# Performance work log

Measured on AMD Instinct MI355X. Metric: run time of the kernel, lower is better.

Reference implementation:

```python
import jax, jax.numpy as jnp
import numpy as np

TIMESCALE = 10.0   # NeuralODE init kwarg
N_MAX = 48         # static upper bound on number of constant-size Dopri5 steps
B, D, H = 8192, 128, 128


def _mlp(y, W1, b1, W2, b2):
    # autonomous dynamics f(x): tanh MLP, applied along last dim
    return jnp.tanh(y @ W1 + b1) @ W2 + b2


def _dopri5_step(y, dt, f):
    # classic Dormand-Prince 5(4) tableau; autonomous f, so c_i unused
    k1 = f(y)
    k2 = f(y + dt * (1.0 / 5.0 * k1))
    k3 = f(y + dt * (3.0 / 40.0 * k1 + 9.0 / 40.0 * k2))
    k4 = f(y + dt * (44.0 / 45.0 * k1 - 56.0 / 15.0 * k2 + 32.0 / 9.0 * k3))
    k5 = f(y + dt * (19372.0 / 6561.0 * k1 - 25360.0 / 2187.0 * k2
                     + 64448.0 / 6561.0 * k3 - 212.0 / 729.0 * k4))
    k6 = f(y + dt * (9017.0 / 3168.0 * k1 - 355.0 / 33.0 * k2
                     + 46732.0 / 5247.0 * k3 + 49.0 / 176.0 * k4
                     - 5103.0 / 18656.0 * k5))
    return y + dt * (35.0 / 384.0 * k1 + 500.0 / 1113.0 * k3
                     + 125.0 / 192.0 * k4 - 2187.0 / 6784.0 * k5
                     + 11.0 / 84.0 * k6)


def _initial_step_size(y0, f0, f, order=4, rtol=1.4e-8, atol=1.4e-8):
    # faithful port of NeuralODE.initial_step_size (Hairer heuristic)
    scale = atol + jnp.abs(y0) * rtol
    d0 = jnp.linalg.norm(y0 / scale)
    d1 = jnp.linalg.norm(f0 / scale)
    h0 = jnp.where((d0 < 1e-5) | (d1 < 1e-5), 1e-6, 0.01 * d0 / d1)
    y1 = y0 + h0 * f0
    f1 = f(y1)
    d2 = jnp.linalg.norm((f1 - f0) / scale) / h0
    h1 = jnp.where((d1 <= 1e-15) & (d2 <= 1e-15),
                   jnp.maximum(1e-6, h0 * 1e-3),
                   (0.01 / (d1 + d2)) ** (1.0 / (order + 1.0)))
    return jnp.minimum(100.0 * h0, h1)


def setup_inputs() -> dict:
    key = jax.random.key(0)
    k0, k1, k2 = jax.random.split(key, 3)
    x = jax.random.normal(k0, (B, D), jnp.float32)
    W1 = jax.random.normal(k1, (D, H), jnp.float32) * (1.0 / D ** 0.5)
    b1 = jnp.zeros((H,), jnp.float32)
    W2 = jax.random.normal(k2, (H, D), jnp.float32) * (1.0 / H ** 0.5)
    b2 = jnp.zeros((D,), jnp.float32)
    t = jnp.ones((1,), jnp.float32)
    return {"t": t, "x": x, "W1": W1, "b1": b1, "W2": W2, "b2": b2}


def reference(t, x, W1, b1, W2, b2):
    f = lambda y: _mlp(y, W1, b1, W2, b2)
    # dt0 from the first state row, exactly as the original (x[0, :])
    dt0 = _initial_step_size(x[0], f(x[0]), f)
    T = t[0] / TIMESCALE  # linspace(0, t/timescale, 2) -> ts = [0, T]

    # diffrax default ConstantStepSize: fixed-dt Dopri5 until t reaches T.
    # Static-length scan with dt clamped to the remaining interval; once
    # t == T, dt == 0 and the step is skipped via lax.cond.
    step = jax.checkpoint(
        lambda y, dt: jax.lax.cond(dt > 0.0,
                                   lambda a: _dopri5_step(a, dt, f),
                                   lambda a: a, y))

    def body(carry, _):
        tt, y = carry
        dt = jnp.clip(T - tt, 0.0, dt0)
        return (tt + dt, step(y, dt)), None

    (_, yT), _ = jax.lax.scan(body, (jnp.zeros((), jnp.float32), x), None,
                              length=N_MAX)
    # SaveAt(ts=[0, T]) -> ys has leading axis n_samples=2
    return jnp.stack([x, yT])
```

## Files before the change

### kernel.cpp

```cpp
#include <hip/hip_runtime.h>


typedef __attribute__((ext_vector_type(8))) short short8;
typedef __attribute__((ext_vector_type(4))) float f32x4;

#define SL 136

__device__ __forceinline__ short f2bf(float f) {
  union { float f; unsigned u; } v; v.f = f;
  return (short)((v.u + 0x8000u) >> 16);
}

__device__ __forceinline__ float fast_tanh(float x) {
  float e = __expf(2.0f * x);
  return 1.0f - __fdividef(2.0f, e + 1.0f);
}

__global__ __launch_bounds__(512, 4)
void node_kernel(const float* __restrict__ tptr, const float* __restrict__ x,
                 const float* __restrict__ W1, const float* __restrict__ b1,
                 const float* __restrict__ W2, const float* __restrict__ b2,
                 float* __restrict__ out) {
  const int tid  = threadIdx.x;
  const int lane = tid & 63;
  const int ct   = tid >> 6;
  const int q    = lane >> 4;
  const int colL = lane & 15;
  const int n    = ct * 16 + colL;
  const int blockRow = blockIdx.x * 16;

  __shared__ short A1[16][SL];
  __shared__ short A2[16][SL];
  __shared__ float sred[512];
  __shared__ float spart[4][128];
  __shared__ float srowY[128], srowH[128], srowF[128], srowY2[128], srowF2[128], sscale[128];

  short8 w1f[4], w2f[4];
  const float b1c = b1[n], b2c = b2[n];
#pragma unroll
  for (int kt = 0; kt < 4; ++kt) {
    short8 v1, v2;
#pragma unroll
    for (int j = 0; j < 8; ++j) {
      const int k = kt * 32 + q * 8 + j;
      v1[j] = f2bf(W1[k * 128 + n]);
      v2[j] = f2bf(W2[k * 128 + n]);
    }
    w1f[kt] = v1; w2f[kt] = v2;
  }

  auto block_sum = [&](float v) -> float {
    sred[tid] = v;
    __syncthreads();
    if (tid < 64) {
      float s = 0.f;
#pragma unroll
      for (int i = 0; i < 8; ++i) s += sred[tid + 64 * i];
#pragma unroll
      for (int o = 32; o > 0; o >>= 1) s += __shfl_down(s, o, 64);
      if (tid == 0) sred[0] = s;
    }
    __syncthreads();
    float r = sred[0];
    __syncthreads();
    return r;
  };

  auto mlp_layer = [&](const float* vin, const float* Wg, const float* bg,
                       float* vout, bool dotanh) {
    const int col = tid & 127, part = tid >> 7;
    float s = 0.f;
    const float* wp = Wg + (part * 32) * 128 + col;
#pragma unroll 8
    for (int j = 0; j < 32; ++j) s += vin[part * 32 + j] * wp[j * 128];
    spart[part][col] = s;
    __syncthreads();
    if (tid < 128) {
      float a = bg[tid] + spart[0][tid] + spart[1][tid] + spart[2][tid] + spart[3][tid];
      vout[tid] = dotanh ? fast_tanh(a) : a;
    }
    __syncthreads();
  };

  if (tid < 128) srowY[tid] = x[tid];
  __syncthreads();
  mlp_layer(srowY, W1, b1, srowH, true);
  mlp_layer(srowH, W2, b2, srowF, false);
  float t0 = 0.f, t1 = 0.f;
  if (tid < 128) {
    float sc = 1.4e-8f + fabsf(srowY[tid]) * 1.4e-8f;
    sscale[tid] = sc;
    float a = srowY[tid] / sc; t0 = a * a;
    float bq = srowF[tid] / sc; t1 = bq * bq;
  }
  float d0 = sqrtf(block_sum(t0));
  float d1 = sqrtf(block_sum(t1));
  float h0 = (d0 < 1e-5f || d1 < 1e-5f) ? 1e-6f : 0.01f * d0 / d1;
  if (tid < 128) srowY2[tid] = srowY[tid] + h0 * srowF[tid];
  __syncthreads();
  mlp_layer(srowY2, W1, b1, srowH, true);
  mlp_layer(srowH, W2, b2, srowF2, false);
  float t2 = 0.f;
  if (tid < 128) { float a = (srowF2[tid] - srowF[tid]) / sscale[tid]; t2 = a * a; }
  float d2 = sqrtf(block_sum(t2)) / h0;
  float h1 = (d1 <= 1e-15f && d2 <= 1e-15f) ? fmaxf(1e-6f, h0 * 1e-3f)
                                            : powf(0.01f / (d1 + d2), 0.2f);
  const float dt0v = fminf(100.f * h0, h1);

  f32x4 yr;
#pragma unroll
  for (int r = 0; r < 4; ++r) yr[r] = x[(blockRow + q * 4 + r) * 128 + n];

  short* wr1 = &A1[q * 4][n];
  short* wr2 = &A2[q * 4][n];
  const short* rd1 = &A1[colL][q * 8];
  const short* rd2 = &A2[colL][q * 8];

  auto evalF = [&](f32x4 yin) -> f32x4 {
#pragma unroll
    for (int r = 0; r < 4; ++r) wr1[r * SL] = f2bf(yin[r]);
    __syncthreads();
    f32x4 acc = {b1c, b1c, b1c, b1c};
#pragma unroll
    for (int kt = 0; kt < 4; ++kt)
      acc = __builtin_amdgcn_mfma_f32_16x16x32_bf16(
          *(const short8*)(rd1 + kt * 32), w1f[kt], acc, 0, 0, 0);
#pragma unroll
    for (int r = 0; r < 4; ++r) wr2[r * SL] = f2bf(fast_tanh(acc[r]));
    __syncthreads();
    f32x4 accF = {b2c, b2c, b2c, b2c};
#pragma unroll
    for (int kt = 0; kt < 4; ++kt)
      accF = __builtin_amdgcn_mfma_f32_16x16x32_bf16(
          *(const short8*)(rd2 + kt * 32), w2f[kt], accF, 0, 0, 0);
    return accF;
  };

  const float T = tptr[0] / 10.0f;
  float tt = 0.f;

#pragma unroll 1
  for (int it = 0; it < 48; ++it) {
    float dt = fminf(fmaxf(T - tt, 0.f), dt0v);
    if (dt > 0.f) {
      f32x4 k1 = evalF(yr);
      f32x4 k2 = evalF(yr + dt * (0.2f * k1));
      f32x4 k3 = evalF(yr + dt * (0.075f * k1 + 0.225f * k2));
      f32x4 k4 = evalF(yr + dt * (0.9777777777777777f * k1 - 3.7333333333333334f * k2
                                + 3.5555555555555554f * k3));
      f32x4 k5 = evalF(yr + dt * (2.9525986892242035f * k1 - 11.595793324188385f * k2
                                + 9.822892851699436f * k3 - 0.2908093278463649f * k4));
      f32x4 k6 = evalF(yr + dt * (2.8462752525252526f * k1 - 10.757575757575758f * k2
                                + 8.906422717743473f * k3 + 0.2784090909090909f * k4
                                - 0.27351165254237287f * k5));
      yr = yr + dt * (0.0911458333333333f * k1 + 0.449236298292902f * k3
                    + 0.6510416666666666f * k4 - 0.32237617924528303f * k5
                    + 0.13095238095238096f * k6);
    }
    tt += dt;
  }

  {
    const float4* x4 = (const float4*)(x + blockRow * 128);
    float4* o4 = (float4*)(out + blockRow * 128);
    o4[tid] = x4[tid];
    float* oy = out + 8192 * 128;
#pragma unroll
    for (int r = 0; r < 4; ++r)
      oy[(blockRow + q * 4 + r) * 128 + n] = yr[r];
  }
}

extern "C" void kernel_launch(void* const* d_in, const int* in_sizes, int n_in,
                              void* d_out, int out_size, void* d_ws, size_t ws_size,
                              hipStream_t stream) {
  const float* t  = (const float*)d_in[0];
  const float* x  = (const float*)d_in[1];
  const float* W1 = (const float*)d_in[2];
  const float* b1 = (const float*)d_in[3];
  const float* W2 = (const float*)d_in[4];
  const float* b2 = (const float*)d_in[5];
  float* out = (float*)d_out;
  node_kernel<<<dim3(512), dim3(512), 0, stream>>>(t, x, W1, b1, W2, b2, out);
}
```

Before: 168.3 us.

## Halve block size, give each wave two feature tiles, and transpose MFMA operands

```diff
diff --git a/kernel.cpp b/kernel.cpp
--- a/kernel.cpp
+++ b/kernel.cpp
@@ -11,51 +11,59 @@
   return (short)((v.u + 0x8000u) >> 16);
 }
 
+__device__ __forceinline__ unsigned pack2bf(float lo, float hi) {
+  union { float f; unsigned u; } a, b; a.f = lo; b.f = hi;
+  return __builtin_amdgcn_perm(b.u + 0x8000u, a.u + 0x8000u, 0x07060302u);
+}
+
 __device__ __forceinline__ float fast_tanh(float x) {
   float e = __expf(2.0f * x);
   return 1.0f - __fdividef(2.0f, e + 1.0f);
 }
 
-__global__ __launch_bounds__(512, 4)
+__global__ __launch_bounds__(256, 2)
 void node_kernel(const float* __restrict__ tptr, const float* __restrict__ x,
                  const float* __restrict__ W1, const float* __restrict__ b1,
                  const float* __restrict__ W2, const float* __restrict__ b2,
                  float* __restrict__ out) {
   const int tid  = threadIdx.x;
   const int lane = tid & 63;
-  const int ct   = tid >> 6;
+  const int w    = tid >> 6;
   const int q    = lane >> 4;
-  const int colL = lane & 15;
-  const int n    = ct * 16 + colL;
+  const int mL   = lane & 15;
   const int blockRow = blockIdx.x * 16;
 
-  __shared__ short A1[16][SL];
-  __shared__ short A2[16][SL];
-  __shared__ float sred[512];
-  __shared__ float spart[4][128];
+  __shared__ short Yb[16 * SL];
+  __shared__ short Tb[16 * SL];
+  __shared__ float sred[256];
+  __shared__ float spart[2][128];
   __shared__ float srowY[128], srowH[128], srowF[128], srowY2[128], srowF2[128], sscale[128];
 
-  short8 w1f[4], w2f[4];
-  const float b1c = b1[n], b2c = b2[n];
-#pragma unroll
-  for (int kt = 0; kt < 4; ++kt) {
-    short8 v1, v2;
-#pragma unroll
-    for (int j = 0; j < 8; ++j) {
-      const int k = kt * 32 + q * 8 + j;
-      v1[j] = f2bf(W1[k * 128 + n]);
-      v2[j] = f2bf(W2[k * 128 + n]);
-    }
-    w1f[kt] = v1; w2f[kt] = v2;
+  short8 w1t[2][4], w2t[2][4];
+  f32x4 b1v[2], b2v[2];
+#pragma unroll
+  for (int s = 0; s < 2; ++s) {
+    const int ft = (2 * w + s) * 16;
+#pragma unroll
+    for (int r = 0; r < 4; ++r) { b1v[s][r] = b1[ft + q * 4 + r]; b2v[s][r] = b2[ft + q * 4 + r]; }
+#pragma unroll
+    for (int kt = 0; kt < 4; ++kt) {
+      short8 v1, v2;
+#pragma unroll
+      for (int j = 0; j < 8; ++j) {
+        const int k = kt * 32 + q * 8 + j;
+        v1[j] = f2bf(W1[k * 128 + ft + mL]);
+        v2[j] = f2bf(W2[k * 128 + ft + mL]);
+      }
+      w1t[s][kt] = v1; w2t[s][kt] = v2;
+    }
   }
 
   auto block_sum = [&](float v) -> float {
     sred[tid] = v;
     __syncthreads();
     if (tid < 64) {
-      float s = 0.f;
-#pragma unroll
-      for (int i = 0; i < 8; ++i) s += sred[tid + 64 * i];
+      float s = sred[tid] + sred[tid + 64] + sred[tid + 128] + sred[tid + 192];
 #pragma unroll
       for (int o = 32; o > 0; o >>= 1) s += __shfl_down(s, o, 64);
       if (tid == 0) sred[0] = s;
@@ -70,13 +78,13 @@
                        float* vout, bool dotanh) {
     const int col = tid & 127, part = tid >> 7;
     float s = 0.f;
-    const float* wp = Wg + (part * 32) * 128 + col;
+    const float* wp = Wg + (part * 64) * 128 + col;
 #pragma unroll 8
-    for (int j = 0; j < 32; ++j) s += vin[part * 32 + j] * wp[j * 128];
+    for (int j = 0; j < 64; ++j) s += vin[part * 64 + j] * wp[j * 128];
     spart[part][col] = s;
     __syncthreads();
     if (tid < 128) {
-      float a = bg[tid] + spart[0][tid] + spart[1][tid] + spart[2][tid] + spart[3][tid];
+      float a = bg[tid] + spart[0][tid] + spart[1][tid];
       vout[tid] = dotanh ? fast_tanh(a) : a;
     }
     __syncthreads();
@@ -107,55 +115,90 @@
                                             : powf(0.01f / (d1 + d2), 0.2f);
   const float dt0v = fminf(100.f * h0, h1);
 
-  f32x4 yr;
-#pragma unroll
-  for (int r = 0; r < 4; ++r) yr[r] = x[(blockRow + q * 4 + r) * 128 + n];
-
-  short* wr1 = &A1[q * 4][n];
-  short* wr2 = &A2[q * 4][n];
-  const short* rd1 = &A1[colL][q * 8];
-  const short* rd2 = &A2[colL][q * 8];
-
-  auto evalF = [&](f32x4 yin) -> f32x4 {
-#pragma unroll
-    for (int r = 0; r < 4; ++r) wr1[r * SL] = f2bf(yin[r]);
-    __syncthreads();
-    f32x4 acc = {b1c, b1c, b1c, b1c};
-#pragma unroll
-    for (int kt = 0; kt < 4; ++kt)
-      acc = __builtin_amdgcn_mfma_f32_16x16x32_bf16(
-          *(const short8*)(rd1 + kt * 32), w1f[kt], acc, 0, 0, 0);
-#pragma unroll
-    for (int r = 0; r < 4; ++r) wr2[r * SL] = f2bf(fast_tanh(acc[r]));
-    __syncthreads();
-    f32x4 accF = {b2c, b2c, b2c, b2c};
-#pragma unroll
-    for (int kt = 0; kt < 4; ++kt)
-      accF = __builtin_amdgcn_mfma_f32_16x16x32_bf16(
-          *(const short8*)(rd2 + kt * 32), w2f[kt], accF, 0, 0, 0);
-    return accF;
+  f32x4 yr[2];
+#pragma unroll
+  for (int s = 0; s < 2; ++s)
+    yr[s] = *(const f32x4*)&x[(blockRow + mL) * 128 + (2 * w + s) * 16 + q * 4];
+
+  const int rowOff = mL * SL;
+  const int wrOff0 = rowOff + (2 * w) * 16 + q * 4;
+  const int wrOff1 = wrOff0 + 16;
+  const int rdOff  = rowOff + q * 8;
+
+  auto evalF = [&](const f32x4* yin, f32x4* kout) {
+    *(uint2*)&Yb[wrOff0] = uint2{pack2bf(yin[0][0], yin[0][1]), pack2bf(yin[0][2], yin[0][3])};
+    *(uint2*)&Yb[wrOff1] = uint2{pack2bf(yin[1][0], yin[1][1]), pack2bf(yin[1][2], yin[1][3])};
+    __syncthreads();
+    f32x4 acc0 = b1v[0], acc1 = b1v[1];
+    short8 rb0 = *(const short8*)&Yb[rdOff];
+    short8 rb1 = *(const short8*)&Yb[rdOff + 32];
+    short8 rb2 = *(const short8*)&Yb[rdOff + 64];
+    short8 rb3 = *(const short8*)&Yb[rdOff + 96];
+    acc0 = __builtin_amdgcn_mfma_f32_16x16x32_bf16(w1t[0][0], rb0, acc0, 0, 0, 0);
+    acc1 = __builtin_amdgcn_mfma_f32_16x16x32_bf16(w1t[1][0], rb0, acc1, 0, 0, 0);
+    acc0 = __builtin_amdgcn_mfma_f32_16x16x32_bf16(w1t[0][1], rb1, acc0, 0, 0, 0);
+    acc1 = __builtin_amdgcn_mfma_f32_16x16x32_bf16(w1t[1][1], rb1, acc1, 0, 0, 0);
+    acc0 = __builtin_amdgcn_mfma_f32_16x16x32_bf16(w1t[0][2], rb2, acc0, 0, 0, 0);
+    acc1 = __builtin_amdgcn_mfma_f32_16x16x32_bf16(w1t[1][2], rb2, acc1, 0, 0, 0);
+    acc0 = __builtin_amdgcn_mfma_f32_16x16x32_bf16(w1t[0][3], rb3, acc0, 0, 0, 0);
+    acc1 = __builtin_amdgcn_mfma_f32_16x16x32_bf16(w1t[1][3], rb3, acc1, 0, 0, 0);
+    *(uint2*)&Tb[wrOff0] = uint2{pack2bf(fast_tanh(acc0[0]), fast_tanh(acc0[1])),
+                                 pack2bf(fast_tanh(acc0[2]), fast_tanh(acc0[3]))};
+    *(uint2*)&Tb[wrOff1] = uint2{pack2bf(fast_tanh(acc1[0]), fast_tanh(acc1[1])),
+                                 pack2bf(fast_tanh(acc1[2]), fast_tanh(acc1[3]))};
+    __syncthreads();
+    f32x4 accF0 = b2v[0], accF1 = b2v[1];
+    short8 tb0 = *(const short8*)&Tb[rdOff];
+    short8 tb1 = *(const short8*)&Tb[rdOff + 32];
+    short8 tb2 = *(const short8*)&Tb[rdOff + 64];
+    short8 tb3 = *(const short8*)&Tb[rdOff + 96];
+    accF0 = __builtin_amdgcn_mfma_f32_16x16x32_bf16(w2t[0][0], tb0, accF0, 0, 0, 0);
+    accF1 = __builtin_amdgcn_mfma_f32_16x16x32_bf16(w2t[1][0], tb0, accF1, 0, 0, 0);
+    accF0 = __builtin_amdgcn_mfma_f32_16x16x32_bf16(w2t[0][1], tb1, accF0, 0, 0, 0);
+    accF1 = __builtin_amdgcn_mfma_f32_16x16x32_bf16(w2t[1][1], tb1, accF1, 0, 0, 0);
+    accF0 = __builtin_amdgcn_mfma_f32_16x16x32_bf16(w2t[0][2], tb2, accF0, 0, 0, 0);
+    accF1 = __builtin_amdgcn_mfma_f32_16x16x32_bf16(w2t[1][2], tb2, accF1, 0, 0, 0);
+    accF0 = __builtin_amdgcn_mfma_f32_16x16x32_bf16(w2t[0][3], tb3, accF0, 0, 0, 0);
+    accF1 = __builtin_amdgcn_mfma_f32_16x16x32_bf16(w2t[1][3], tb3, accF1, 0, 0, 0);
+    kout[0] = accF0; kout[1] = accF1;
   };
 
   const float T = tptr[0] / 10.0f;
   float tt = 0.f;
+  f32x4 k1[2], k2[2], k3[2], k4[2], k5[2], k6[2], yv[2];
 
 #pragma unroll 1
   for (int it = 0; it < 48; ++it) {
     float dt = fminf(fmaxf(T - tt, 0.f), dt0v);
     if (dt > 0.f) {
-      f32x4 k1 = evalF(yr);
-      f32x4 k2 = evalF(yr + dt * (0.2f * k1));
-      f32x4 k3 = evalF(yr + dt * (0.075f * k1 + 0.225f * k2));
-      f32x4 k4 = evalF(yr + dt * (0.9777777777777777f * k1 - 3.7333333333333334f * k2
-                                + 3.5555555555555554f * k3));
-      f32x4 k5 = evalF(yr + dt * (2.9525986892242035f * k1 - 11.595793324188385f * k2
-                                + 9.822892851699436f * k3 - 0.2908093278463649f * k4));
-      f32x4 k6 = evalF(yr + dt * (2.8462752525252526f * k1 - 10.757575757575758f * k2
-                                + 8.906422717743473f * k3 + 0.2784090909090909f * k4
-                                - 0.27351165254237287f * k5));
-      yr = yr + dt * (0.0911458333333333f * k1 + 0.449236298292902f * k3
-                    + 0.6510416666666666f * k4 - 0.32237617924528303f * k5
-                    + 0.13095238095238096f * k6);
+      evalF(yr, k1);
+#pragma unroll
+      for (int s = 0; s < 2; ++s) yv[s] = yr[s] + dt * (0.2f * k1[s]);
+      evalF(yv, k2);
+#pragma unroll
+      for (int s = 0; s < 2; ++s) yv[s] = yr[s] + dt * (0.075f * k1[s] + 0.225f * k2[s]);
+      evalF(yv, k3);
+#pragma unroll
+      for (int s = 0; s < 2; ++s)
+        yv[s] = yr[s] + dt * (0.9777777777777777f * k1[s] - 3.7333333333333334f * k2[s]
+                            + 3.5555555555555554f * k3[s]);
+      evalF(yv, k4);
+#pragma unroll
+      for (int s = 0; s < 2; ++s)
+        yv[s] = yr[s] + dt * (2.9525986892242035f * k1[s] - 11.595793324188385f * k2[s]
+                            + 9.822892851699436f * k3[s] - 0.2908093278463649f * k4[s]);
+      evalF(yv, k5);
+#pragma unroll
+      for (int s = 0; s < 2; ++s)
+        yv[s] = yr[s] + dt * (2.8462752525252526f * k1[s] - 10.757575757575758f * k2[s]
+                            + 8.906422717743473f * k3[s] + 0.2784090909090909f * k4[s]
+                            - 0.27351165254237287f * k5[s]);
+      evalF(yv, k6);
+#pragma unroll
+      for (int s = 0; s < 2; ++s)
+        yr[s] = yr[s] + dt * (0.0911458333333333f * k1[s] + 0.449236298292902f * k3[s]
+                            + 0.6510416666666666f * k4[s] - 0.32237617924528303f * k5[s]
+                            + 0.13095238095238096f * k6[s]);
     }
     tt += dt;
   }
@@ -163,11 +206,12 @@
   {
     const float4* x4 = (const float4*)(x + blockRow * 128);
     float4* o4 = (float4*)(out + blockRow * 128);
-    o4[tid] = x4[tid];
+#pragma unroll
+    for (int i = 0; i < 2; ++i) o4[tid + 256 * i] = x4[tid + 256 * i];
     float* oy = out + 8192 * 128;
 #pragma unroll
-    for (int r = 0; r < 4; ++r)
-      oy[(blockRow + q * 4 + r) * 128 + n] = yr[r];
+    for (int s = 0; s < 2; ++s)
+      *(f32x4*)&oy[(blockRow + mL) * 128 + (2 * w + s) * 16 + q * 4] = yr[s];
   }
 }
 
@@ -181,5 +225,5 @@
   const float* W2 = (const float*)d_in[4];
   const float* b2 = (const float*)d_in[5];
   float* out = (float*)d_out;
-  node_kernel<<<dim3(512), dim3(512), 0, stream>>>(t, x, W1, b1, W2, b2, out);
-}
+  node_kernel<<<dim3(512), dim3(256), 0, stream>>>(t, x, W1, b1, W2, b2, out);
+}
```

Result: slower. 172.7 us (+2.6%).
